# Performance work log

Hardware: AMD Instinct MI355X
Metric: run time of the kernel (lower is better)

The kernel has to match this reference:

```python
import jax, jax.numpy as jnp
import numpy as np

E = 384      # EMBEDDING_SIZE
DFF = 1536
H = 6        # NUM_HEADS
D = E // H   # ATTN_DIM_SIZE = 64
T = 256      # SEQ_LEN
L = 6        # NUM_BLOCKS
V = 65       # VOCAB_SIZE
NPOS = 10000.0
B = 128


def _pos_encoding():
    i = jnp.arange(T, dtype=jnp.float32)[:, None]
    k = jnp.arange(E // 2, dtype=jnp.float32)[None, :]
    ang = i / jnp.power(NPOS, 2.0 * k / E)   # [T, E/2]
    pe = jnp.zeros((T, E), dtype=jnp.float32)
    pe = pe.at[:, 0::2].set(jnp.sin(ang))
    pe = pe.at[:, 1::2].set(jnp.cos(ang))
    return pe


def setup_inputs() -> dict:
    key = jax.random.key(0)
    ks = jax.random.split(key, 24)
    s = 0.02
    n = lambda k, shp: (jax.random.normal(k, shp, dtype=jnp.float32) * s)
    inp = {
        'tokens': jax.random.randint(ks[0], (B, T), 0, V),
        'pos_enc': _pos_encoding(),
        'emb': n(ks[1], (V, E)),
        # stacked per-layer params [L, ...]; weights stored as (in, out)
        'Wq': n(ks[2], (L, E, E)), 'bq': jnp.zeros((L, E)),
        'Wk': n(ks[3], (L, E, E)), 'bk': jnp.zeros((L, E)),
        'Wv': n(ks[4], (L, E, E)), 'bv': jnp.zeros((L, E)),
        'Wo': n(ks[5], (L, E, E)), 'bo': jnp.zeros((L, E)),
        'ln1_g': jnp.ones((L, E)), 'ln1_b': jnp.zeros((L, E)),
        'W1': n(ks[6], (L, E, DFF)), 'c1': jnp.zeros((L, DFF)),
        'W2': n(ks[7], (L, DFF, E)), 'c2': jnp.zeros((L, E)),
        'ln2_g': jnp.ones((L, E)), 'ln2_b': jnp.zeros((L, E)),
        'Wl': n(ks[8], (E, V)), 'bl': jnp.zeros((V,)),
    }
    return inp


def _layer_norm(x, g, b, eps=1e-5):
    mu = jnp.mean(x, axis=-1, keepdims=True)
    var = jnp.mean((x - mu) ** 2, axis=-1, keepdims=True)
    return (x - mu) * jax.lax.rsqrt(var + eps) * g + b


def _decoder(tokens, pos_enc, emb, Wq, bq, Wk, bk, Wv, bv, Wo, bo,
             ln1_g, ln1_b, W1, c1, W2, c2, ln2_g, ln2_b, Wl, bl):
    b_, t_ = tokens.shape
    x = emb[tokens] + pos_enc[None, :t_, :]            # [B,T,E]
    causal = jnp.tril(jnp.ones((t_, t_), dtype=bool)) # tril mask
    scale = D ** (-0.5)

    def block(x, p):
        (wq, bq_, wk, bk_, wv, bv_, wo, bo_, g1, be1, w1, c1_, w2, c2_, g2, be2) = p
        h = _layer_norm(x, g1, be1)
        q = (h @ wq + bq_).reshape(b_, t_, H, D)
        k = (h @ wk + bk_).reshape(b_, t_, H, D)
        v = (h @ wv + bv_).reshape(b_, t_, H, D)
        scores = jnp.einsum('bqhd,bkhd->bhqk', q, k) * scale
        scores = jnp.where(causal[None, None], scores, -jnp.inf)
        attn = jax.nn.softmax(scores, axis=-1)
        o = jnp.einsum('bhqk,bkhd->bqhd', attn, v).reshape(b_, t_, E)
        x = x + (o @ wo + bo_)
        h2 = _layer_norm(x, g2, be2)
        x = x + (jax.nn.relu(h2 @ w1 + c1_) @ w2 + c2_)
        return x, None

    params = (Wq, bq, Wk, bk, Wv, bv, Wo, bo, ln1_g, ln1_b, W1, c1, W2, c2, ln2_g, ln2_b)
    x, _ = jax.lax.scan(block, x, params)
    return x @ Wl + bl                                 # [B,T,V]


def reference(tokens, pos_enc, emb, Wq, bq, Wk, bk, Wv, bv, Wo, bo,
              ln1_g, ln1_b, W1, c1, W2, c2, ln2_g, ln2_b, Wl, bl):
    return _decoder(tokens, pos_enc, emb, Wq, bq, Wk, bk, Wv, bv, Wo, bo,
                    ln1_g, ln1_b, W1, c1, W2, c2, ln2_g, ln2_b, Wl, bl)
```

## Files before the change

### kernel.cpp

```cpp
#include <hip/hip_runtime.h>
#include <hip/hip_bf16.h>
#include <stdint.h>

constexpr int E   = 384;
constexpr int DFF = 1536;
constexpr int NH  = 6;
constexpr int HD  = 64;
constexpr int T   = 256;
constexpr int NL  = 6;
constexpr int NV  = 65;
constexpr int BB  = 128;
constexpr int MTOT = BB * T;
constexpr int CB  = 32;

typedef __bf16 bf16;
typedef __attribute__((ext_vector_type(8))) __bf16 bf16x8;
typedef __attribute__((ext_vector_type(4))) __bf16 bf16x4;
typedef __attribute__((ext_vector_type(4))) float floatx4;

__device__ __forceinline__ void gload_lds16(const void* g, void* l) {
    __builtin_amdgcn_global_load_lds(
        (const __attribute__((address_space(1))) void*)g,
        (__attribute__((address_space(3))) void*)l, 16, 0, 0);
}

#define GBM 256
#define GBN 128
#define GBK 64

template <int MODE, int SWAP>
__device__ __forceinline__ void gemm_body(
    char* AsB,
    const bf16* __restrict__ A, int lda,
    const bf16* __restrict__ Bf,
    const float* __restrict__ bias,
    void* __restrict__ Cv, void* __restrict__ Cv2, int ldc,
    int nt, int mt, int Nvalid, int K, int relu)
{
    int tid = threadIdx.x;
    int lane = tid & 63;
    int wid = tid >> 6;
    int wr = wid >> 1, wc = wid & 1;
    int lq = lane >> 4, lr = lane & 15;

    const bf16* Ab = A + (long)mt * GBM * lda;

    int srow = tid >> 3;
    int slot = tid & 7;
    int skc  = (slot ^ (srow & 7)) * 8;
    const bf16* Arow = Ab + (long)srow * lda + skc;
    const long a2 = 64 * (long)lda;
    int wofs = wid * 1024;

    int nk = K / GBK;
    int nks = K / 32;
    const bf16* Bq = Bf + ((long)(nt * 8 + wc * 4) * nks) * 512 + lane * 8;

    floatx4 acc[4][4];
#pragma unroll
    for (int i = 0; i < 4; i++)
#pragma unroll
        for (int j = 0; j < 4; j++) acc[i][j] = floatx4{0.f, 0.f, 0.f, 0.f};

    const char* rp0 = AsB + (wr * 64 + lr) * 128;
    int rx0 = (lq * 16) ^ ((lr & 7) << 4);

#pragma unroll
    for (int g = 0; g < 4; g++)
        gload_lds16(Arow + g * a2, AsB + wofs + g * 8192);
    asm volatile("s_waitcnt vmcnt(0)" ::: "memory");
    __syncthreads();

    for (int ki = 0; ki < nk; ki++) {
        int ib = ki & 1;
        bf16x8 bb[4];
#pragma unroll
        for (int ni = 0; ni < 4; ni++)
            bb[ni] = *(const bf16x8*)(Bq + ((long)ni * nks + 2 * ki) * 512);
        if (ki + 1 < nk) {
            long koff = (long)(ki + 1) * GBK;
            char* base = AsB + (1 - ib) * 32768 + wofs;
#pragma unroll
            for (int g = 0; g < 4; g++)
                gload_lds16(Arow + g * a2 + koff, base + g * 8192);
        }
        const char* rp = rp0 + ib * 32768;

        bf16x8 af[4];
#pragma unroll
        for (int mi = 0; mi < 4; mi++)
            af[mi] = *(const bf16x8*)(rp + mi * 2048 + rx0);
#pragma unroll
        for (int mi = 0; mi < 4; mi++)
#pragma unroll
            for (int ni = 0; ni < 4; ni++)
                acc[mi][ni] = SWAP
                    ? __builtin_amdgcn_mfma_f32_16x16x32_bf16(bb[ni], af[mi], acc[mi][ni], 0, 0, 0)
                    : __builtin_amdgcn_mfma_f32_16x16x32_bf16(af[mi], bb[ni], acc[mi][ni], 0, 0, 0);
#pragma unroll
        for (int ni = 0; ni < 4; ni++)
            bb[ni] = *(const bf16x8*)(Bq + ((long)ni * nks + 2 * ki + 1) * 512);
#pragma unroll
        for (int mi = 0; mi < 4; mi++)
            af[mi] = *(const bf16x8*)(rp + mi * 2048 + (rx0 ^ 64));
#pragma unroll
        for (int mi = 0; mi < 4; mi++)
#pragma unroll
            for (int ni = 0; ni < 4; ni++)
                acc[mi][ni] = SWAP
                    ? __builtin_amdgcn_mfma_f32_16x16x32_bf16(bb[ni], af[mi], acc[mi][ni], 0, 0, 0)
                    : __builtin_amdgcn_mfma_f32_16x16x32_bf16(af[mi], bb[ni], acc[mi][ni], 0, 0, 0);
        __syncthreads();
    }

    int m0 = mt * GBM, n0 = nt * GBN;
#pragma unroll
    for (int mi = 0; mi < 4; mi++) {
#pragma unroll
        for (int ni = 0; ni < 4; ni++) {
            floatx4 v = acc[mi][ni];
            if (SWAP) {
                int rowL = m0 + wr * 64 + mi * 16 + lr;
                int col0 = n0 + wc * 64 + ni * 16 + lq * 4;
                if (MODE == 5) {
                    bf16x4 pv;
#pragma unroll
                    for (int r = 0; r < 4; r++) pv[r] = (bf16)(v[r] + bias[col0 + r]);
                    *(bf16x4*)((bf16*)Cv + (long)rowL * 768 + col0) = pv;
                } else if (MODE == 1) {
                    bf16* Cp = (bf16*)Cv;
                    bf16x4* ptr = (bf16x4*)(Cp + (long)rowL * ldc + col0);
                    bf16x4 old = *ptr;
                    bf16x4 pv;
#pragma unroll
                    for (int r = 0; r < 4; r++)
                        pv[r] = (bf16)((float)old[r] + v[r] + bias[col0 + r]);
                    *ptr = pv;
                } else if (MODE == 4) {
                    float* Cp = (float*)Cv;
#pragma unroll
                    for (int r = 0; r < 4; r++)
                        if (col0 + r < Nvalid)
                            Cp[(long)rowL * ldc + col0 + r] = v[r] + bias[col0 + r];
                } else {
                    if (col0 < Nvalid) {
                        bf16x4 pv;
#pragma unroll
                        for (int r = 0; r < 4; r++) {
                            float x = v[r] + (bias ? bias[col0 + r] : 0.f);
                            if (relu) x = fmaxf(x, 0.f);
                            pv[r] = (bf16)x;
                        }
                        *(bf16x4*)((bf16*)Cv + (long)rowL * ldc + col0) = pv;
                    }
                }
            } else {
                int row0 = m0 + wr * 64 + mi * 16 + lq * 4;
                int colL = n0 + wc * 64 + ni * 16 + lr;
                float bv = bias[colL];
                bf16x4 pv;
#pragma unroll
                for (int r = 0; r < 4; r++) pv[r] = (bf16)(v[r] + bv);
                int bidx = row0 >> 8, pos = row0 & 255, e = colL - 768;
                *(bf16x4*)((bf16*)Cv2 + (long)bidx * (E * T) + (long)e * T + pos) = pv;
            }
        }
    }
}

template <int MODE>
__global__ __launch_bounds__(512, 4) void k_gemm(
    const bf16* __restrict__ A, int lda,
    const bf16* __restrict__ Bf,
    const float* __restrict__ bias,
    void* __restrict__ Cv, void* __restrict__ Cv2, int ldc,
    int Mtiles, int Ntiles, int Nvalid, int K,
    int relu)
{
    __shared__ __align__(16) char AsB[2 * 32768];

    int nb = gridDim.x;
    int per = nb >> 3;
    int bphys = blockIdx.x;
    int bid = (bphys & 7) * per + (bphys >> 3);

    int nt = bid % Ntiles;
    int mt = bid / Ntiles;

    if (MODE == 5 && nt >= 6)
        gemm_body<5, 0>(AsB, A, lda, Bf, bias, Cv, Cv2, ldc, nt, mt, Nvalid, K, relu);
    else
        gemm_body<MODE, 1>(AsB, A, lda, Bf, bias, Cv, Cv2, ldc, nt, mt, Nvalid, K, relu);
}

__global__ __launch_bounds__(256) void k_attn(
    const bf16* __restrict__ qk, const bf16* __restrict__ vt,
    bf16* __restrict__ o)
{
    int nb = gridDim.x;
    int per = nb >> 3;
    int bphys = blockIdx.x;
    int bid = (bphys & 7) * per + (bphys >> 3);

    int qt = bid & 3; bid >>= 2;
    int h = bid % NH; int b = bid / NH;
    int tid = threadIdx.x;
    int lane = tid & 63;
    int w = tid >> 6;
    int lq = lane >> 4;
    int lr = lane & 15;

    __shared__ __align__(16) bf16 Ks[256 * 72];
    __shared__ __align__(16) bf16 Vs[64 * 264];

    const bf16* qbase = qk + (long)(b * T + qt * 64 + w * 16) * 768 + h * 64;
    const bf16* kbase = qk + (long)(b * T) * 768 + 384 + h * 64;
    const bf16* vbase = vt + ((long)b * E + h * 64) * T;

#pragma unroll
    for (int i = 0; i < 8; i++) {
        int idx = i * 256 + tid;
        int row = idx >> 3, off = (idx & 7) * 8;
        *(bf16x8*)(&Ks[row * 72 + off]) = *(const bf16x8*)(kbase + (long)row * 768 + off);
    }
#pragma unroll
    for (int i = 0; i < 8; i++) {
        int idx = i * 256 + tid;
        int row = idx >> 5, off = (idx & 31) * 8;
        *(bf16x8*)(&Vs[row * 264 + off]) = *(const bf16x8*)(vbase + (long)row * 256 + off);
    }

    bf16x8 aq0 = *(const bf16x8*)(qbase + (long)lr * 768 + lq * 8);
    bf16x8 aq1 = *(const bf16x8*)(qbase + (long)lr * 768 + 32 + lq * 8);

    __syncthreads();

    const int ntmax = qt * 4 + 3;
    floatx4 zero = {0.f, 0.f, 0.f, 0.f};
    floatx4 s[16];
#pragma unroll
    for (int nt = 0; nt < 16; nt++) s[nt] = zero;

#pragma unroll
    for (int nt = 0; nt < 16; nt++) {
        if (nt <= ntmax) {
            const bf16* kp = &Ks[(nt * 16 + lr) * 72 + lq * 8];
            bf16x8 b0 = *(const bf16x8*)(kp);
            bf16x8 b1 = *(const bf16x8*)(kp + 32);
            s[nt] = __builtin_amdgcn_mfma_f32_16x16x32_bf16(aq0, b0, s[nt], 0, 0, 0);
            s[nt] = __builtin_amdgcn_mfma_f32_16x16x32_bf16(aq1, b1, s[nt], 0, 0, 0);
        }
    }

    int trow0 = qt * 64 + w * 16 + lq * 4;
    float m4[4] = {-3e38f, -3e38f, -3e38f, -3e38f};
#pragma unroll
    for (int nt = 0; nt < 16; nt++) {
        if (nt <= ntmax) {
            int tc = nt * 16 + lr;
#pragma unroll
            for (int r = 0; r < 4; r++) {
                float v = s[nt][r] * 0.125f;
                if (tc > trow0 + r) v = -3e38f;
                s[nt][r] = v;
                m4[r] = fmaxf(m4[r], v);
            }
        }
    }
#pragma unroll
    for (int r = 0; r < 4; r++) {
#pragma unroll
        for (int off = 1; off < 16; off <<= 1)
            m4[r] = fmaxf(m4[r], __shfl_xor(m4[r], off, 64));
    }

    float l4[4] = {0.f, 0.f, 0.f, 0.f};
#pragma unroll
    for (int nt = 0; nt < 16; nt++) {
        if (nt <= ntmax) {
#pragma unroll
            for (int r = 0; r < 4; r++) {
                float pv = __expf(s[nt][r] - m4[r]);
                l4[r] += pv;
                s[nt][r] = pv;
            }
        }
    }
#pragma unroll
    for (int r = 0; r < 4; r++) {
#pragma unroll
        for (int off = 1; off < 16; off <<= 1)
            l4[r] += __shfl_xor(l4[r], off, 64);
    }

    __syncthreads();

    bf16* P = Ks + w * (16 * 264);
#pragma unroll
    for (int nt = 0; nt < 16; nt++) {
        if (nt <= ntmax) {
#pragma unroll
            for (int r = 0; r < 4; r++)
                P[(lq * 4 + r) * 264 + nt * 16 + lr] = (bf16)s[nt][r];
        }
    }

    floatx4 oacc[4];
#pragma unroll
    for (int nd = 0; nd < 4; nd++) oacc[nd] = zero;
    const int kkmax = 2 * (qt + 1);
#pragma unroll
    for (int kk = 0; kk < 8; kk++) {
        if (kk < kkmax) {
            bf16x8 ap = *(const bf16x8*)(&P[lr * 264 + kk * 32 + lq * 8]);
#pragma unroll
            for (int nd = 0; nd < 4; nd++) {
                bf16x8 bv = *(const bf16x8*)(&Vs[(nd * 16 + lr) * 264 + kk * 32 + lq * 8]);
                oacc[nd] = __builtin_amdgcn_mfma_f32_16x16x32_bf16(ap, bv, oacc[nd], 0, 0, 0);
            }
        }
    }

#pragma unroll
    for (int r = 0; r < 4; r++) {
        float inv = 1.0f / l4[r];
        long rowg = (long)b * T + trow0 + r;
#pragma unroll
        for (int nd = 0; nd < 4; nd++) {
            o[rowg * E + h * 64 + nd * 16 + lr] = (bf16)(oacc[nd][r] * inv);
        }
    }
}

__global__ void k_ln(const bf16* __restrict__ x, const float* __restrict__ g,
                     const float* __restrict__ b, bf16* __restrict__ h) {
    int row = blockIdx.x * 4 + (threadIdx.x >> 6);
    int lane = threadIdx.x & 63;
    const bf16* xr = x + (long)row * E;
    float v[6];
    float s = 0.f;
#pragma unroll
    for (int i = 0; i < 6; i++) { v[i] = (float)xr[lane + 64 * i]; s += v[i]; }
#pragma unroll
    for (int o = 1; o < 64; o <<= 1) s += __shfl_xor(s, o, 64);
    float mu = s * (1.0f / E);
    float q = 0.f;
#pragma unroll
    for (int i = 0; i < 6; i++) { float d = v[i] - mu; q += d * d; }
#pragma unroll
    for (int o = 1; o < 64; o <<= 1) q += __shfl_xor(q, o, 64);
    float rs = rsqrtf(q * (1.0f / E) + 1e-5f);
    bf16* hr = h + (long)row * E;
#pragma unroll
    for (int i = 0; i < 6; i++) {
        int c = lane + 64 * i;
        hr[c] = (bf16)((v[i] - mu) * rs * g[c] + b[c]);
    }
}

__global__ void k_transpose_frag(const float* __restrict__ W, bf16* __restrict__ Wf,
                                 int K, int N, int NPAD) {
    long idx = (long)blockIdx.x * 256 + threadIdx.x;
    long per = (long)NPAD * K;
    int l = (int)(idx / per);
    long r = idx - (long)l * per;
    int j = (int)(r & 7); r >>= 3;
    int lane = (int)(r & 63); r >>= 6;
    int nks = K / 32;
    int ks = (int)(r % nks);
    int c16 = (int)(r / nks);
    int col = c16 * 16 + (lane & 15);
    int k = ks * 32 + (lane >> 4) * 8 + j;
    Wf[idx] = (col < N) ? (bf16)W[((long)l * K + k) * N + col] : (bf16)0.0f;
}

__global__ void k_transpose_qkv_frag(const float* __restrict__ Wq, const float* __restrict__ Wk,
                                     const float* __restrict__ Wv, bf16* __restrict__ Wf) {
    long idx = (long)blockIdx.x * 256 + threadIdx.x;
    long per = (long)1152 * E;
    int l = (int)(idx / per);
    long r = idx - (long)l * per;
    int j = (int)(r & 7); r >>= 3;
    int lane = (int)(r & 63); r >>= 6;
    int nks = E / 32;
    int ks = (int)(r % nks);
    int c16 = (int)(r / nks);
    int col = c16 * 16 + (lane & 15);
    int k = ks * 32 + (lane >> 4) * 8 + j;
    const float* src;
    int cc;
    if (col < 384)      { src = Wq; cc = col; }
    else if (col < 768) { src = Wk; cc = col - 384; }
    else                { src = Wv; cc = col - 768; }
    Wf[idx] = (bf16)src[((long)l * E + k) * E + cc];
}

__global__ void k_bias_qkv(const float* __restrict__ bq, const float* __restrict__ bk,
                           const float* __restrict__ bv, float* __restrict__ bqkv) {
    int idx = blockIdx.x * 256 + threadIdx.x;
    int l = idx / 1152;
    int j = idx - l * 1152;
    const float* src;
    int jj;
    if (j < 384)      { src = bq; jj = j; }
    else if (j < 768) { src = bk; jj = j - 384; }
    else              { src = bv; jj = j - 768; }
    bqkv[idx] = src[l * E + jj];
}

__global__ void k_embed(const int* __restrict__ tokens, const float* __restrict__ pos,
                        const float* __restrict__ emb, bf16* __restrict__ x) {
    long idx = (long)blockIdx.x * 256 + threadIdx.x;
    int e = (int)(idx % E);
    long bt = idx / E;
    int t = (int)(bt % T);
    int tok = tokens[bt];
    x[idx] = (bf16)(emb[(long)tok * E + e] + pos[(long)t * E + e]);
}

extern "C" void kernel_launch(void* const* d_in, const int* in_sizes, int n_in,
                              void* d_out, int out_size, void* d_ws, size_t ws_size,
                              hipStream_t stream) {
    const int*   tokens = (const int*)d_in[0];
    const float* pos  = (const float*)d_in[1];
    const float* emb  = (const float*)d_in[2];
    const float* Wq   = (const float*)d_in[3];
    const float* bq   = (const float*)d_in[4];
    const float* Wk   = (const float*)d_in[5];
    const float* bk   = (const float*)d_in[6];
    const float* Wv   = (const float*)d_in[7];
    const float* bv   = (const float*)d_in[8];
    const float* Wo   = (const float*)d_in[9];
    const float* bo   = (const float*)d_in[10];
    const float* g1   = (const float*)d_in[11];
    const float* be1  = (const float*)d_in[12];
    const float* W1   = (const float*)d_in[13];
    const float* c1   = (const float*)d_in[14];
    const float* W2   = (const float*)d_in[15];
    const float* c2   = (const float*)d_in[16];
    const float* g2   = (const float*)d_in[17];
    const float* be2  = (const float*)d_in[18];
    const float* Wl   = (const float*)d_in[19];
    const float* bl   = (const float*)d_in[20];

    char* p = (char*)d_ws;
    bf16* x  = (bf16*)p;   p += (long)MTOT * E * 2;
    bf16* h  = (bf16*)p;   p += (long)MTOT * E * 2;
    bf16* qk = (bf16*)p;   p += (long)MTOT * 768 * 2;
    bf16* vt = (bf16*)p;   p += (long)BB * E * T * 2;
    bf16* SP = (bf16*)p;   p += (long)CB * NH * T * T * 2;
    bf16* WqkvF = (bf16*)p; p += (long)NL * 1152 * E * 2;
    bf16* WoF = (bf16*)p;  p += (long)NL * E * E * 2;
    bf16* W1F = (bf16*)p;  p += (long)NL * DFF * E * 2;
    bf16* W2F = (bf16*)p;  p += (long)NL * E * DFF * 2;
    bf16* WlF = (bf16*)p;  p += (long)128 * E * 2;
    float* bqkv = (float*)p; p += (long)NL * 1152 * 4;
    bf16* mid = qk;
    bf16* o   = h;
    (void)SP;

    k_transpose_qkv_frag<<<(NL * 1152 * E) / 256, 256, 0, stream>>>(Wq, Wk, Wv, WqkvF);
    k_transpose_frag<<<(NL * E * E) / 256, 256, 0, stream>>>(Wo, WoF, E, E, E);
    k_transpose_frag<<<(NL * DFF * E) / 256, 256, 0, stream>>>(W1, W1F, E, DFF, DFF);
    k_transpose_frag<<<(NL * E * DFF) / 256, 256, 0, stream>>>(W2, W2F, DFF, E, E);
    k_transpose_frag<<<(128 * E) / 256, 256, 0, stream>>>(Wl, WlF, E, NV, 128);
    k_bias_qkv<<<(NL * 1152) / 256, 256, 0, stream>>>(bq, bk, bv, bqkv);

    k_embed<<<(MTOT * E) / 256, 256, 0, stream>>>(tokens, pos, emb, x);

    for (int l = 0; l < NL; l++) {
        k_ln<<<MTOT / 4, 256, 0, stream>>>(x, g1 + l * E, be1 + l * E, h);
        k_gemm<5><<<128 * 9, 512, 0, stream>>>(h, E, WqkvF + (long)l * 1152 * E,
                                               bqkv + l * 1152, qk, vt, 0,
                                               128, 9, 1152, E, 0);
        k_attn<<<BB * NH * 4, 256, 0, stream>>>(qk, vt, o);
        k_gemm<1><<<128 * 3, 512, 0, stream>>>(o, E, WoF + (long)l * E * E,
                                               bo + l * E, x, nullptr, E,
                                               128, 3, E, E, 0);
        k_ln<<<MTOT / 4, 256, 0, stream>>>(x, g2 + l * E, be2 + l * E, h);
        k_gemm<0><<<128 * 12, 512, 0, stream>>>(h, E, W1F + (long)l * DFF * E,
                                                c1 + l * DFF, mid, nullptr, DFF,
                                                128, 12, DFF, E, 1);
        k_gemm<1><<<128 * 3, 512, 0, stream>>>(mid, DFF, W2F + (long)l * E * DFF,
                                               c2 + l * E, x, nullptr, E,
                                               128, 3, E, DFF, 0);
    }

    k_gemm<4><<<128 * 1, 512, 0, stream>>>(x, E, WlF,
                                           bl, d_out, nullptr, NV,
                                           128, 1, NV, E, 0);
}
```

Baseline: 1.893 ms.

## Triple-buffer GEMM A tiles with K=32 steps and templated block height

Rewrites the GEMM mainloop to step K by 32, with a three-stage LDS ring buffer that prefetches A two steps ahead. Each step uses a single barrier with partial vmcnt waits and raises wave priority around the MFMA cluster. The row-tile height becomes a template parameter. The narrow N=384 GEMMs (Wo, W2) and the vocab projection now run 128-row tiles with 256 threads, doubling their block count to fill more CUs. The risks are more barriers per K, a new swizzle layout, and smaller tiles that reuse each B fragment less.

```diff
diff --git a/kernel.cpp b/kernel.cpp
--- a/kernel.cpp
+++ b/kernel.cpp
@@ -24,11 +24,9 @@
         (__attribute__((address_space(3))) void*)l, 16, 0, 0);
 }
 
-#define GBM 256
 #define GBN 128
-#define GBK 64
-
-template <int MODE, int SWAP>
+
+template <int MODE, int SWAP, int W>
 __device__ __forceinline__ void gemm_body(
     char* AsB,
     const bf16* __restrict__ A, int lda,
@@ -37,22 +35,27 @@
     void* __restrict__ Cv, void* __restrict__ Cv2, int ldc,
     int nt, int mt, int Nvalid, int K, int relu)
 {
+    constexpr int BM   = W * 32;
+    constexpr int ABUF = BM * 64;
+
     int tid = threadIdx.x;
     int lane = tid & 63;
     int wid = tid >> 6;
     int wr = wid >> 1, wc = wid & 1;
     int lq = lane >> 4, lr = lane & 15;
 
-    const bf16* Ab = A + (long)mt * GBM * lda;
-
-    int srow = tid >> 3;
-    int slot = tid & 7;
-    int skc  = (slot ^ (srow & 7)) * 8;
-    const bf16* Arow = Ab + (long)srow * lda + skc;
-    const long a2 = 64 * (long)lda;
-    int wofs = wid * 1024;
-
-    int nk = K / GBK;
+    const bf16* Ab = A + (long)mt * BM * lda;
+
+    int rp0 = wid * 8 + (lane >> 3);
+    int s   = lane & 7;
+    int sp  = s ^ (rp0 & 7);
+    int rowA = 2 * rp0 + (sp >> 2);
+    int kOff = (sp & 3) * 8;
+    const bf16* srcA0 = Ab + (long)rowA * lda + kOff;
+    const bf16* srcA1 = srcA0 + (long)(BM / 2) * lda;
+    int dst0 = wid * 1024;
+    int dst1 = W * 1024 + wid * 1024;
+
     int nks = K / 32;
     const bf16* Bq = Bf + ((long)(nt * 8 + wc * 4) * nks) * 512 + lane * 8;
 
@@ -62,34 +65,38 @@
 #pragma unroll
         for (int j = 0; j < 4; j++) acc[i][j] = floatx4{0.f, 0.f, 0.f, 0.f};
 
-    const char* rp0 = AsB + (wr * 64 + lr) * 128;
-    int rx0 = (lq * 16) ^ ((lr & 7) << 4);
-
-#pragma unroll
-    for (int g = 0; g < 4; g++)
-        gload_lds16(Arow + g * a2, AsB + wofs + g * 8192);
-    asm volatile("s_waitcnt vmcnt(0)" ::: "memory");
-    __syncthreads();
-
-    for (int ki = 0; ki < nk; ki++) {
-        int ib = ki & 1;
+    int afo = (wr * 32 + (lr >> 1)) * 128 +
+              (((((lr & 1) << 2) | lq) ^ (lr >> 1)) << 4);
+
+    gload_lds16(srcA0, AsB + dst0);
+    gload_lds16(srcA1, AsB + dst1);
+    if (nks > 1) {
+        gload_lds16(srcA0 + 32, AsB + ABUF + dst0);
+        gload_lds16(srcA1 + 32, AsB + ABUF + dst1);
+        asm volatile("s_waitcnt vmcnt(2)" ::: "memory");
+    } else {
+        asm volatile("s_waitcnt vmcnt(0)" ::: "memory");
+    }
+    __builtin_amdgcn_s_barrier();
+
+    int o0 = 0, o1 = ABUF, o2 = 2 * ABUF;
+    for (int ki = 0; ki < nks; ++ki) {
         bf16x8 bb[4];
 #pragma unroll
         for (int ni = 0; ni < 4; ni++)
-            bb[ni] = *(const bf16x8*)(Bq + ((long)ni * nks + 2 * ki) * 512);
-        if (ki + 1 < nk) {
-            long koff = (long)(ki + 1) * GBK;
-            char* base = AsB + (1 - ib) * 32768 + wofs;
-#pragma unroll
-            for (int g = 0; g < 4; g++)
-                gload_lds16(Arow + g * a2 + koff, base + g * 8192);
-        }
-        const char* rp = rp0 + ib * 32768;
-
+            bb[ni] = *(const bf16x8*)(Bq + ((long)ni * nks + ki) * 512);
+        __builtin_amdgcn_sched_barrier(0);
+        if (ki + 2 < nks) {
+            long ko = (long)(ki + 2) * 32;
+            gload_lds16(srcA0 + ko, AsB + o2 + dst0);
+            gload_lds16(srcA1 + ko, AsB + o2 + dst1);
+        }
+        const char* rp = AsB + o0 + afo;
         bf16x8 af[4];
 #pragma unroll
         for (int mi = 0; mi < 4; mi++)
-            af[mi] = *(const bf16x8*)(rp + mi * 2048 + rx0);
+            af[mi] = *(const bf16x8*)(rp + mi * 1024);
+        __builtin_amdgcn_s_setprio(1);
 #pragma unroll
         for (int mi = 0; mi < 4; mi++)
 #pragma unroll
@@ -97,23 +104,18 @@
                 acc[mi][ni] = SWAP
                     ? __builtin_amdgcn_mfma_f32_16x16x32_bf16(bb[ni], af[mi], acc[mi][ni], 0, 0, 0)
                     : __builtin_amdgcn_mfma_f32_16x16x32_bf16(af[mi], bb[ni], acc[mi][ni], 0, 0, 0);
-#pragma unroll
-        for (int ni = 0; ni < 4; ni++)
-            bb[ni] = *(const bf16x8*)(Bq + ((long)ni * nks + 2 * ki + 1) * 512);
-#pragma unroll
-        for (int mi = 0; mi < 4; mi++)
-            af[mi] = *(const bf16x8*)(rp + mi * 2048 + (rx0 ^ 64));
-#pragma unroll
-        for (int mi = 0; mi < 4; mi++)
-#pragma unroll
-            for (int ni = 0; ni < 4; ni++)
-                acc[mi][ni] = SWAP
-                    ? __builtin_amdgcn_mfma_f32_16x16x32_bf16(bb[ni], af[mi], acc[mi][ni], 0, 0, 0)
-                    : __builtin_amdgcn_mfma_f32_16x16x32_bf16(af[mi], bb[ni], acc[mi][ni], 0, 0, 0);
-        __syncthreads();
-    }
-
-    int m0 = mt * GBM, n0 = nt * GBN;
+        __builtin_amdgcn_s_setprio(0);
+        if (ki + 1 < nks) {
+            if (ki + 2 < nks)
+                asm volatile("s_waitcnt vmcnt(2) lgkmcnt(0)" ::: "memory");
+            else
+                asm volatile("s_waitcnt vmcnt(0) lgkmcnt(0)" ::: "memory");
+            __builtin_amdgcn_s_barrier();
+        }
+        int t = o0; o0 = o1; o1 = o2; o2 = t;
+    }
+
+    int m0 = mt * BM, n0 = nt * GBN;
 #pragma unroll
     for (int mi = 0; mi < 4; mi++) {
 #pragma unroll
@@ -168,8 +170,8 @@
     }
 }
 
-template <int MODE>
-__global__ __launch_bounds__(512, 4) void k_gemm(
+template <int MODE, int W>
+__global__ __launch_bounds__(W * 64, 4) void k_gemm(
     const bf16* __restrict__ A, int lda,
     const bf16* __restrict__ Bf,
     const float* __restrict__ bias,
@@ -177,7 +179,7 @@
     int Mtiles, int Ntiles, int Nvalid, int K,
     int relu)
 {
-    __shared__ __align__(16) char AsB[2 * 32768];
+    __shared__ __align__(16) char AsB[3 * W * 32 * 64];
 
     int nb = gridDim.x;
     int per = nb >> 3;
@@ -188,9 +190,9 @@
     int mt = bid / Ntiles;
 
     if (MODE == 5 && nt >= 6)
-        gemm_body<5, 0>(AsB, A, lda, Bf, bias, Cv, Cv2, ldc, nt, mt, Nvalid, K, relu);
+        gemm_body<5, 0, W>(AsB, A, lda, Bf, bias, Cv, Cv2, ldc, nt, mt, Nvalid, K, relu);
     else
-        gemm_body<MODE, 1>(AsB, A, lda, Bf, bias, Cv, Cv2, ldc, nt, mt, Nvalid, K, relu);
+        gemm_body<MODE, 1, W>(AsB, A, lda, Bf, bias, Cv, Cv2, ldc, nt, mt, Nvalid, K, relu);
 }
 
 __global__ __launch_bounds__(256) void k_attn(
@@ -470,23 +472,23 @@
 
     for (int l = 0; l < NL; l++) {
         k_ln<<<MTOT / 4, 256, 0, stream>>>(x, g1 + l * E, be1 + l * E, h);
-        k_gemm<5><<<128 * 9, 512, 0, stream>>>(h, E, WqkvF + (long)l * 1152 * E,
-                                               bqkv + l * 1152, qk, vt, 0,
-                                               128, 9, 1152, E, 0);
+        k_gemm<5, 8><<<128 * 9, 512, 0, stream>>>(h, E, WqkvF + (long)l * 1152 * E,
+                                                  bqkv + l * 1152, qk, vt, 0,
+                                                  128, 9, 1152, E, 0);
         k_attn<<<BB * NH * 4, 256, 0, stream>>>(qk, vt, o);
-        k_gemm<1><<<128 * 3, 512, 0, stream>>>(o, E, WoF + (long)l * E * E,
-                                               bo + l * E, x, nullptr, E,
-                                               128, 3, E, E, 0);
+        k_gemm<1, 4><<<256 * 3, 256, 0, stream>>>(o, E, WoF + (long)l * E * E,
+                                                  bo + l * E, x, nullptr, E,
+                                                  256, 3, E, E, 0);
         k_ln<<<MTOT / 4, 256, 0, stream>>>(x, g2 + l * E, be2 + l * E, h);
-        k_gemm<0><<<128 * 12, 512, 0, stream>>>(h, E, W1F + (long)l * DFF * E,
-                                                c1 + l * DFF, mid, nullptr, DFF,
-                                                128, 12, DFF, E, 1);
-        k_gemm<1><<<128 * 3, 512, 0, stream>>>(mid, DFF, W2F + (long)l * E * DFF,
-                                               c2 + l * E, x, nullptr, E,
-                                               128, 3, E, DFF, 0);
-    }
-
-    k_gemm<4><<<128 * 1, 512, 0, stream>>>(x, E, WlF,
-                                           bl, d_out, nullptr, NV,
-                                           128, 1, NV, E, 0);
-}
+        k_gemm<0, 8><<<128 * 12, 512, 0, stream>>>(h, E, W1F + (long)l * DFF * E,
+                                                   c1 + l * DFF, mid, nullptr, DFF,
+                                                   128, 12, DFF, E, 1);
+        k_gemm<1, 4><<<256 * 3, 256, 0, stream>>>(mid, DFF, W2F + (long)l * E * DFF,
+                                                  c2 + l * E, x, nullptr, E,
+                                                  256, 3, E, DFF, 0);
+    }
+
+    k_gemm<4, 4><<<256 * 1, 256, 0, stream>>>(x, E, WlF,
+                                              bl, d_out, nullptr, NV,
+                                              256, 1, NV, E, 0);
+}
```

Measured after the change: 1.814 ms. 1.04x faster.
